# Kernel tuning notes

Measured on AMD Instinct MI355X. Metric: run time of the kernel, lower is better.

## Reference

```python
import jax, jax.numpy as jnp
import numpy as np

NEIGHBOR_K = 3

def setup_inputs() -> dict:
    key = jax.random.key(0)
    k1, k2 = jax.random.split(key)
    query_fea = jax.random.normal(k1, (8, 75, 121, 640), dtype=jnp.float32)
    support_fea = jax.random.normal(k2, (8, 5, 5, 121, 640), dtype=jnp.float32)
    return {"query_fea": query_fea, "support_fea": support_fea}

def reference(query_fea, support_fea):
    # query_fea: [b, n_wq, patch_num, dim]
    # support_fea: [b, way, shot, patch_num, dim]
    b, way, shot, pn, dim = support_fea.shape
    sup = support_fea.reshape(b, way, shot * pn, dim)  # [b, way, S, dim]
    # inner products between every query patch and every support patch
    # sim: [b, n_wq, way, patch_num, S]
    sim = jnp.einsum('bqpd,bwsd->bqwps', query_fea, sup)
    # top-k over support patches (last axis), then mean over all topk values
    topk = jax.lax.top_k(sim, NEIGHBOR_K)[0]  # [b, n_wq, way, patch_num, k]
    return jnp.mean(topk, axis=(-2, -1))  # [b, n_wq, way]
```

## Files before the change

kernel.cpp:

```cpp
#include <hip/hip_runtime.h>
#include <hip/hip_bf16.h>

#define BATCH 8
#define NQ    75
#define WAY   5
#define PN    121
#define DIM   640
#define SSZ   605
#define TOPK  3

#define KCH 10
#define NCH 5

#define NQTILES 6000
#define NSTILES 2000
#define WSQ_BYTES ((size_t)NQTILES * 16384)
#define WS_NEED   ((size_t)(NQTILES + NSTILES) * 16384)

typedef __attribute__((ext_vector_type(8))) short   short8;
typedef __attribute__((ext_vector_type(8))) __bf16  bf16x8;
typedef __attribute__((ext_vector_type(4))) float   f32x4;

__device__ inline unsigned short f2bf(float f) {
  unsigned u = __builtin_bit_cast(unsigned, f);
  return (unsigned short)((u + 0x7fffu + ((u >> 16) & 1u)) >> 16);
}
__device__ inline unsigned pk2(float lo, float hi) {
  return (unsigned)f2bf(lo) | ((unsigned)f2bf(hi) << 16);
}

__device__ inline void ins3(float &a, float &b, float &c, float v) {
  float na  = fmaxf(a, v);
  float nb  = __builtin_amdgcn_fmed3f(v, a, b);
  float nc2 = __builtin_amdgcn_fmed3f(v, b, c);
  a = na; b = nb; c = nc2;
}

__device__ inline void async_copy16(const void* g, void* l) {
  __builtin_amdgcn_global_load_lds(
      (const __attribute__((address_space(1))) unsigned int*)g,
      (__attribute__((address_space(3))) unsigned int*)l, 16, 0, 0);
}

__global__ __launch_bounds__(256) void cvt_pack(const float* __restrict__ qf,
                                                const float* __restrict__ sf,
                                                uint4* __restrict__ wq,
                                                uint4* __restrict__ wsp) {
  const int blk = blockIdx.x;
  const float* src;
  uint4* dst;
  int nrows;
  if (blk < NQTILES) {
    int kc = blk % KCH;
    int bq = blk / KCH;
    src = qf + (size_t)bq * PN * DIM + kc * 64;
    dst = wq + (size_t)blk * 1024;
    nrows = PN;
  } else {
    int t  = blk - NQTILES;
    int kc = t % KCH;
    int u  = t / KCH;
    int nc = u % NCH;
    int bw = u / NCH;
    src = sf + ((size_t)bw * SSZ + nc * 128) * DIM + kc * 64;
    dst = wsp + (size_t)t * 1024;
    nrows = SSZ - nc * 128; if (nrows > 128) nrows = 128;
  }
  #pragma unroll
  for (int i = 0; i < 4; ++i) {
    int ch  = i * 256 + threadIdx.x;
    int p   = ch & 7;
    int row = ch >> 3;
    int c   = p ^ (row & 7);
    uint4 o = make_uint4(0u, 0u, 0u, 0u);
    if (row < nrows) {
      const float* g = src + (size_t)row * DIM + c * 8;
      float4 v0 = reinterpret_cast<const float4*>(g)[0];
      float4 v1 = reinterpret_cast<const float4*>(g)[1];
      o.x = pk2(v0.x, v0.y); o.y = pk2(v0.z, v0.w);
      o.z = pk2(v1.x, v1.y); o.w = pk2(v1.z, v1.w);
    }
    dst[ch] = o;
  }
}

__global__ __launch_bounds__(256, 3) void lpc_main(
    const char* __restrict__ wq,
    const char* __restrict__ wsp,
    float* __restrict__ out)
{
  __shared__ char Qs[16384];
  __shared__ char Ss[16384];
  __shared__ float red[4];

  const int sbid = blockIdx.x;
  const int bid  = (sbid & 7) * (NQ * WAY) + (sbid >> 3);

  const int w   = bid % WAY;
  const int bq  = bid / WAY;
  const int b   = bid / (WAY * NQ);

  const char* Qtiles = wq  + (size_t)bq * KCH * 16384;
  const char* Stiles = wsp + (size_t)(b * WAY + w) * NCH * KCH * 16384;

  const int tid  = threadIdx.x;
  const int lane = tid & 63;
  const int wv   = tid >> 6;
  const int l15  = lane & 15;
  const int quad = lane >> 4;
  const int mrow0 = (wv >> 1) * 64;
  const int ncol0 = (wv & 1) * 64;

  const int sw16 = (l15 & 7) * 16;
  const int cp0  = (quad * 16) ^ sw16;
  const int cp1  = ((4 + quad) * 16) ^ sw16;

  const char* qb = Qs + (mrow0 + l15) * 128;
  const char* sb = Ss + (ncol0 + l15) * 128;

  float t3a[4][4], t3b[4][4], t3c[4][4];
  #pragma unroll
  for (int mt = 0; mt < 4; ++mt)
    #pragma unroll
    for (int r = 0; r < 4; ++r) {
      t3a[mt][r] = -3.0e38f; t3b[mt][r] = -3.0e38f; t3c[mt][r] = -3.0e38f;
    }

  for (int nc = 0; nc < NCH; ++nc) {
    f32x4 acc[4][4];
    #pragma unroll
    for (int mt = 0; mt < 4; ++mt)
      #pragma unroll
      for (int nt = 0; nt < 4; ++nt)
        acc[mt][nt] = (f32x4){0.f, 0.f, 0.f, 0.f};

    #pragma unroll 1
    for (int kc = 0; kc < KCH; ++kc) {
      __syncthreads();
      {
        const char* qsl = Qtiles + (size_t)kc * 16384;
        const char* ssl = Stiles + ((size_t)nc * KCH + kc) * 16384;
        #pragma unroll
        for (int i = 0; i < 4; ++i) {
          int ch = wv * 4 + i;
          async_copy16(qsl + ch * 1024 + lane * 16, Qs + ch * 1024);
          async_copy16(ssl + ch * 1024 + lane * 16, Ss + ch * 1024);
        }
      }
      __syncthreads();

      #pragma unroll
      for (int kk = 0; kk < 2; ++kk) {
        const int cp = kk ? cp1 : cp0;
        short8 a[4], bf[4];
        #pragma unroll
        for (int mt = 0; mt < 4; ++mt)
          a[mt] = *reinterpret_cast<const short8*>(qb + mt * 2048 + cp);
        #pragma unroll
        for (int nt = 0; nt < 4; ++nt)
          bf[nt] = *reinterpret_cast<const short8*>(sb + nt * 2048 + cp);
        #pragma unroll
        for (int mt = 0; mt < 4; ++mt)
          #pragma unroll
          for (int nt = 0; nt < 4; ++nt)
            acc[mt][nt] = __builtin_amdgcn_mfma_f32_16x16x32_bf16(
                __builtin_bit_cast(bf16x8, a[mt]),
                __builtin_bit_cast(bf16x8, bf[nt]), acc[mt][nt], 0, 0, 0);
      }
    }

    #pragma unroll
    for (int nt = 0; nt < 4; ++nt) {
      int col = nc * 128 + ncol0 + nt * 16 + l15;
      bool valid = col < SSZ;
      #pragma unroll
      for (int mt = 0; mt < 4; ++mt)
        #pragma unroll
        for (int r = 0; r < 4; ++r) {
          float v = valid ? acc[mt][nt][r] : -3.0e38f;
          ins3(t3a[mt][r], t3b[mt][r], t3c[mt][r], v);
        }
    }
  }

  #pragma unroll
  for (int m = 1; m < 16; m <<= 1) {
    #pragma unroll
    for (int mt = 0; mt < 4; ++mt)
      #pragma unroll
      for (int r = 0; r < 4; ++r) {
        float o0 = __shfl_xor(t3a[mt][r], m);
        float o1 = __shfl_xor(t3b[mt][r], m);
        float o2 = __shfl_xor(t3c[mt][r], m);
        ins3(t3a[mt][r], t3b[mt][r], t3c[mt][r], o0);
        ins3(t3a[mt][r], t3b[mt][r], t3c[mt][r], o1);
        ins3(t3a[mt][r], t3b[mt][r], t3c[mt][r], o2);
      }
  }

  float* tb = reinterpret_cast<float*>(Qs);
  __syncthreads();
  if ((wv & 1) == 1 && l15 == 0) {
    #pragma unroll
    for (int mt = 0; mt < 4; ++mt)
      #pragma unroll
      for (int r = 0; r < 4; ++r) {
        int row = mrow0 + mt * 16 + quad * 4 + r;
        tb[row * 3 + 0] = t3a[mt][r];
        tb[row * 3 + 1] = t3b[mt][r];
        tb[row * 3 + 2] = t3c[mt][r];
      }
  }
  __syncthreads();
  if ((wv & 1) == 0 && l15 == 0) {
    #pragma unroll
    for (int mt = 0; mt < 4; ++mt)
      #pragma unroll
      for (int r = 0; r < 4; ++r) {
        int row = mrow0 + mt * 16 + quad * 4 + r;
        ins3(t3a[mt][r], t3b[mt][r], t3c[mt][r], tb[row * 3 + 0]);
        ins3(t3a[mt][r], t3b[mt][r], t3c[mt][r], tb[row * 3 + 1]);
        ins3(t3a[mt][r], t3b[mt][r], t3c[mt][r], tb[row * 3 + 2]);
      }
  }
  __syncthreads();
  if ((wv & 1) == 0 && l15 == 0) {
    #pragma unroll
    for (int mt = 0; mt < 4; ++mt)
      #pragma unroll
      for (int r = 0; r < 4; ++r) {
        int row = mrow0 + mt * 16 + quad * 4 + r;
        tb[row * 3 + 0] = t3a[mt][r];
        tb[row * 3 + 1] = t3b[mt][r];
        tb[row * 3 + 2] = t3c[mt][r];
      }
  }
  __syncthreads();

  float s = 0.f;
  for (int i = tid; i < PN * TOPK; i += 256) s += tb[i];
  #pragma unroll
  for (int off = 32; off > 0; off >>= 1) s += __shfl_down(s, off);
  if (lane == 0) red[wv] = s;
  __syncthreads();
  if (tid == 0)
    out[bid] = (red[0] + red[1] + red[2] + red[3]) * (1.0f / (PN * TOPK));
}

__global__ __launch_bounds__(256) void lpc_fallback(
    const float* __restrict__ qf, const float* __restrict__ sf,
    float* __restrict__ out)
{
  __shared__ short Qst[128][72];
  __shared__ short Sst[64][72];
  __shared__ float Cs[128][67];
  __shared__ float top3[128][TOPK];
  __shared__ float red[4];

  const int bid = blockIdx.x;
  const int w   = bid % WAY;
  const int qi  = (bid / WAY) % NQ;
  const int b   = bid / (WAY * NQ);
  const float* Qb = qf + ((size_t)(b * NQ + qi)) * PN * DIM;
  const float* Sb = sf + ((size_t)(b * WAY + w)) * SSZ * DIM;
  const int tid  = threadIdx.x;
  const int lane = tid & 63;
  const int wv   = tid >> 6;
  const int l15  = lane & 15;
  const int quad = lane >> 4;

  if (tid < 128) { top3[tid][0] = -3.0e38f; top3[tid][1] = -3.0e38f; top3[tid][2] = -3.0e38f; }
  f32x4 acc[2][4];
  for (int nc = 0; nc < 10; ++nc) {
    const int sbase = nc * 64;
    int vn = SSZ - sbase; if (vn > 64) vn = 64;
    #pragma unroll
    for (int mt = 0; mt < 2; ++mt)
      #pragma unroll
      for (int nt = 0; nt < 4; ++nt) acc[mt][nt] = (f32x4){0.f,0.f,0.f,0.f};
    for (int kc = 0; kc < KCH; ++kc) {
      const int kbase = kc * 64;
      __syncthreads();
      #pragma unroll
      for (int i = 0; i < 8; ++i) {
        int lin = i * 256 + tid; int row = lin >> 4; int c4 = lin & 15;
        float4 v = make_float4(0.f,0.f,0.f,0.f);
        if (row < PN) v = *reinterpret_cast<const float4*>(Qb + (size_t)row * DIM + kbase + c4 * 4);
        ushort4 h; h.x=f2bf(v.x); h.y=f2bf(v.y); h.z=f2bf(v.z); h.w=f2bf(v.w);
        *reinterpret_cast<ushort4*>(&Qst[row][c4*4]) = h;
      }
      #pragma unroll
      for (int i = 0; i < 4; ++i) {
        int lin = i * 256 + tid; int row = lin >> 4; int c4 = lin & 15;
        int srow = sbase + row;
        float4 v = make_float4(0.f,0.f,0.f,0.f);
        if (srow < SSZ) v = *reinterpret_cast<const float4*>(Sb + (size_t)srow * DIM + kbase + c4 * 4);
        ushort4 h; h.x=f2bf(v.x); h.y=f2bf(v.y); h.z=f2bf(v.z); h.w=f2bf(v.w);
        *reinterpret_cast<ushort4*>(&Sst[row][c4*4]) = h;
      }
      __syncthreads();
      #pragma unroll
      for (int kk = 0; kk < 2; ++kk) {
        bf16x8 a0 = __builtin_bit_cast(bf16x8, *reinterpret_cast<const short8*>(&Qst[wv*32+ 0+l15][kk*32+quad*8]));
        bf16x8 a1 = __builtin_bit_cast(bf16x8, *reinterpret_cast<const short8*>(&Qst[wv*32+16+l15][kk*32+quad*8]));
        #pragma unroll
        for (int nt = 0; nt < 4; ++nt) {
          bf16x8 bb = __builtin_bit_cast(bf16x8, *reinterpret_cast<const short8*>(&Sst[nt*16+l15][kk*32+quad*8]));
          acc[0][nt] = __builtin_amdgcn_mfma_f32_16x16x32_bf16(a0, bb, acc[0][nt], 0,0,0);
          acc[1][nt] = __builtin_amdgcn_mfma_f32_16x16x32_bf16(a1, bb, acc[1][nt], 0,0,0);
        }
      }
    }
    #pragma unroll
    for (int mt = 0; mt < 2; ++mt)
      #pragma unroll
      for (int nt = 0; nt < 4; ++nt)
        #pragma unroll
        for (int r = 0; r < 4; ++r)
          Cs[wv*32+mt*16+quad*4+r][nt*16+l15] = acc[mt][nt][r];
    __syncthreads();
    {
      int row = tid >> 1; int half = tid & 1;
      float a = -3.0e38f, b2 = -3.0e38f, c = -3.0e38f;
      int c0 = half * 32; int cend = c0 + 32; if (cend > vn) cend = vn;
      for (int cc = c0; cc < cend; ++cc) ins3(a, b2, c, Cs[row][cc]);
      float o0 = __shfl_xor(a,1), o1 = __shfl_xor(b2,1), o2 = __shfl_xor(c,1);
      ins3(a,b2,c,o0); ins3(a,b2,c,o1); ins3(a,b2,c,o2);
      if (half == 0) {
        float r0=top3[row][0], r1=top3[row][1], r2=top3[row][2];
        ins3(r0,r1,r2,a); ins3(r0,r1,r2,b2); ins3(r0,r1,r2,c);
        top3[row][0]=r0; top3[row][1]=r1; top3[row][2]=r2;
      }
    }
    __syncthreads();
  }
  float s = 0.f;
  for (int i = tid; i < PN * TOPK; i += 256) s += top3[i/TOPK][i%TOPK];
  #pragma unroll
  for (int off = 32; off > 0; off >>= 1) s += __shfl_down(s, off);
  if (lane == 0) red[wv] = s;
  __syncthreads();
  if (tid == 0) out[bid] = (red[0]+red[1]+red[2]+red[3]) * (1.0f/(PN*TOPK));
}

extern "C" void kernel_launch(void* const* d_in, const int* in_sizes, int n_in,
                              void* d_out, int out_size, void* d_ws, size_t ws_size,
                              hipStream_t stream) {
  const float* qf = (const float*)d_in[0];
  const float* sf = (const float*)d_in[1];
  float* out = (float*)d_out;
  (void)in_sizes; (void)n_in; (void)out_size;

  if (ws_size >= WS_NEED && d_ws != nullptr) {
    uint4* wq  = (uint4*)d_ws;
    uint4* wsp = wq + (size_t)NQTILES * 1024;
    cvt_pack<<<NQTILES + NSTILES, 256, 0, stream>>>(qf, sf, wq, wsp);
    lpc_main<<<BATCH * NQ * WAY, 256, 0, stream>>>((const char*)wq, (const char*)wsp, out);
  } else {
    lpc_fallback<<<BATCH * NQ * WAY, 256, 0, stream>>>(qf, sf, out);
  }
}
```

Before: 627.1 us.

## Double-buffer LDS tiles with async prefetch and flatten the chunk loops

Adds a second LDS buffer for the Q and S tiles so the next K-chunk is fetched asynchronously while MFMAs run on the current one. Full __syncthreads are replaced by explicit vmcnt waits and raw barriers, and MFMA sections are wrapped in s_setprio. The nc/kc loops are flattened into a single linear loop. LDS use doubles to about 64KB per block and launch bounds drop from 3 to 2 blocks per CU, trading occupancy for overlap of loads and compute.

Result: slower. 669.5 us (+6.8%).

```diff
diff --git a/kernel.cpp b/kernel.cpp
--- a/kernel.cpp
+++ b/kernel.cpp
@@ -84,13 +84,13 @@
   }
 }
 
-__global__ __launch_bounds__(256, 3) void lpc_main(
+__global__ __launch_bounds__(256, 2) void lpc_main(
     const char* __restrict__ wq,
     const char* __restrict__ wsp,
     float* __restrict__ out)
 {
-  __shared__ char Qs[16384];
-  __shared__ char Ss[16384];
+  __shared__ char Qs[2][16384];
+  __shared__ char Ss[2][16384];
   __shared__ float red[4];
 
   const int sbid = blockIdx.x;
@@ -115,8 +115,8 @@
   const int cp0  = (quad * 16) ^ sw16;
   const int cp1  = ((4 + quad) * 16) ^ sw16;
 
-  const char* qb = Qs + (mrow0 + l15) * 128;
-  const char* sb = Ss + (ncol0 + l15) * 128;
+  const int qoff = (mrow0 + l15) * 128;
+  const int soff = (ncol0 + l15) * 128;
 
   float t3a[4][4], t3b[4][4], t3c[4][4];
   #pragma unroll
@@ -126,60 +126,99 @@
       t3a[mt][r] = -3.0e38f; t3b[mt][r] = -3.0e38f; t3c[mt][r] = -3.0e38f;
     }
 
-  for (int nc = 0; nc < NCH; ++nc) {
-    f32x4 acc[4][4];
-    #pragma unroll
-    for (int mt = 0; mt < 4; ++mt)
-      #pragma unroll
-      for (int nt = 0; nt < 4; ++nt)
-        acc[mt][nt] = (f32x4){0.f, 0.f, 0.f, 0.f};
-
-    #pragma unroll 1
-    for (int kc = 0; kc < KCH; ++kc) {
-      __syncthreads();
-      {
-        const char* qsl = Qtiles + (size_t)kc * 16384;
-        const char* ssl = Stiles + ((size_t)nc * KCH + kc) * 16384;
-        #pragma unroll
-        for (int i = 0; i < 4; ++i) {
-          int ch = wv * 4 + i;
-          async_copy16(qsl + ch * 1024 + lane * 16, Qs + ch * 1024);
-          async_copy16(ssl + ch * 1024 + lane * 16, Ss + ch * 1024);
-        }
-      }
-      __syncthreads();
-
-      #pragma unroll
-      for (int kk = 0; kk < 2; ++kk) {
-        const int cp = kk ? cp1 : cp0;
-        short8 a[4], bf[4];
-        #pragma unroll
-        for (int mt = 0; mt < 4; ++mt)
-          a[mt] = *reinterpret_cast<const short8*>(qb + mt * 2048 + cp);
+  {
+    #pragma unroll
+    for (int i = 0; i < 4; ++i) {
+      const int ch = wv * 4 + i;
+      const int go = ch * 1024 + lane * 16;
+      async_copy16(Qtiles + go, &Qs[0][ch * 1024]);
+      async_copy16(Stiles + go, &Ss[0][ch * 1024]);
+    }
+    #pragma unroll
+    for (int i = 0; i < 4; ++i) {
+      const int ch = wv * 4 + i;
+      const int go = ch * 1024 + lane * 16;
+      async_copy16(Qtiles + 16384 + go, &Qs[1][ch * 1024]);
+      async_copy16(Stiles + 16384 + go, &Ss[1][ch * 1024]);
+    }
+  }
+
+  f32x4 acc[4][4];
+  int nc = 0;
+  int kc = 0;
+  int kc2 = 2;
+
+  #pragma unroll 1
+  for (int t = 0; t < NCH * KCH; ++t) {
+    const int cur = t & 1;
+
+    if (kc == 0) {
+      #pragma unroll
+      for (int mt = 0; mt < 4; ++mt)
         #pragma unroll
         for (int nt = 0; nt < 4; ++nt)
-          bf[nt] = *reinterpret_cast<const short8*>(sb + nt * 2048 + cp);
+          acc[mt][nt] = (f32x4){0.f, 0.f, 0.f, 0.f};
+    }
+
+    if (t < 49) asm volatile("s_waitcnt vmcnt(8)" ::: "memory");
+    else        asm volatile("s_waitcnt vmcnt(0)" ::: "memory");
+    asm volatile("s_barrier" ::: "memory");
+
+    const char* qb = &Qs[cur][0] + qoff;
+    const char* sb = &Ss[cur][0] + soff;
+
+    __builtin_amdgcn_s_setprio(1);
+    #pragma unroll
+    for (int kk = 0; kk < 2; ++kk) {
+      const int cp = kk ? cp1 : cp0;
+      short8 a[4], bf[4];
+      #pragma unroll
+      for (int mt = 0; mt < 4; ++mt)
+        a[mt] = *reinterpret_cast<const short8*>(qb + mt * 2048 + cp);
+      #pragma unroll
+      for (int nt = 0; nt < 4; ++nt)
+        bf[nt] = *reinterpret_cast<const short8*>(sb + nt * 2048 + cp);
+      #pragma unroll
+      for (int mt = 0; mt < 4; ++mt)
+        #pragma unroll
+        for (int nt = 0; nt < 4; ++nt)
+          acc[mt][nt] = __builtin_amdgcn_mfma_f32_16x16x32_bf16(
+              __builtin_bit_cast(bf16x8, a[mt]),
+              __builtin_bit_cast(bf16x8, bf[nt]), acc[mt][nt], 0, 0, 0);
+    }
+    __builtin_amdgcn_s_setprio(0);
+
+    asm volatile("s_barrier" ::: "memory");
+
+    if (t < 48) {
+      const char* qsl = Qtiles + kc2 * 16384;
+      const char* ssl = Stiles + (size_t)(t + 2) * 16384;
+      #pragma unroll
+      for (int i = 0; i < 4; ++i) {
+        const int ch = wv * 4 + i;
+        const int go = ch * 1024 + lane * 16;
+        async_copy16(qsl + go, &Qs[cur][ch * 1024]);
+        async_copy16(ssl + go, &Ss[cur][ch * 1024]);
+      }
+    }
+    kc2 = (kc2 == 9) ? 0 : kc2 + 1;
+
+    if (kc == 9) {
+      #pragma unroll
+      for (int nt = 0; nt < 4; ++nt) {
+        const int col = nc * 128 + ncol0 + nt * 16 + l15;
+        const bool valid = col < SSZ;
         #pragma unroll
         for (int mt = 0; mt < 4; ++mt)
           #pragma unroll
-          for (int nt = 0; nt < 4; ++nt)
-            acc[mt][nt] = __builtin_amdgcn_mfma_f32_16x16x32_bf16(
-                __builtin_bit_cast(bf16x8, a[mt]),
-                __builtin_bit_cast(bf16x8, bf[nt]), acc[mt][nt], 0, 0, 0);
-      }
-    }
-
-    #pragma unroll
-    for (int nt = 0; nt < 4; ++nt) {
-      int col = nc * 128 + ncol0 + nt * 16 + l15;
-      bool valid = col < SSZ;
-      #pragma unroll
-      for (int mt = 0; mt < 4; ++mt)
-        #pragma unroll
-        for (int r = 0; r < 4; ++r) {
-          float v = valid ? acc[mt][nt][r] : -3.0e38f;
-          ins3(t3a[mt][r], t3b[mt][r], t3c[mt][r], v);
-        }
+          for (int r = 0; r < 4; ++r) {
+            float v = valid ? acc[mt][nt][r] : -3.0e38f;
+            ins3(t3a[mt][r], t3b[mt][r], t3c[mt][r], v);
+          }
+      }
+      ++nc; kc = 0;
+    } else {
+      ++kc;
     }
   }
 
@@ -198,7 +237,7 @@
       }
   }
 
-  float* tb = reinterpret_cast<float*>(Qs);
+  float* tb = reinterpret_cast<float*>(&Qs[0][0]);
   __syncthreads();
   if ((wv & 1) == 1 && l15 == 0) {
     #pragma unroll
```
